# Kernel tuning notes

Measured on AMD Instinct MI355X. Metric: run time of the kernel, lower is better.

The kernel has to match this reference:

```python
import jax, jax.numpy as jnp
import numpy as np

ACT_DIM = 768
DICT_SIZE = 32768
S0 = 4096          # top-level latent size (dict_size // prod(lower sizes))
S1 = 8             # lower_level_latent_sizes[0]
K = 64             # per-token top-k (applied globally as k * batch)


def setup_inputs() -> dict:
    key = jax.random.key(0)
    ks = jax.random.split(key, 7)
    scale_e = 1.0 / np.sqrt(ACT_DIM)
    scale_d = 1.0 / np.sqrt(DICT_SIZE)
    return {
        "x": jax.random.normal(ks[0], (4096, ACT_DIM), dtype=jnp.float32),
        "W0": jax.random.normal(ks[1], (S0, ACT_DIM), dtype=jnp.float32) * scale_e,
        "b0": jnp.zeros((S0,), dtype=jnp.float32),
        "W1": jax.random.normal(ks[2], (DICT_SIZE, ACT_DIM), dtype=jnp.float32) * scale_e,
        "b1": jnp.zeros((DICT_SIZE,), dtype=jnp.float32),
        "Wd": jax.random.normal(ks[3], (ACT_DIM, DICT_SIZE), dtype=jnp.float32) * scale_d,
        "b_dec": jnp.zeros((ACT_DIM,), dtype=jnp.float32),
    }


def reference(x, W0, b0, W1, b1, Wd, b_dec):
    B = x.shape[0]
    x_centered = x - b_dec                                   # [B, D]
    # hierarchical relu encoders
    l0 = jax.nn.relu(x_centered @ W0.T + b0)                 # [B, S0]
    l1 = jax.nn.relu(x_centered @ W1.T + b1)                 # [B, S0*S1]
    # multiplicative gating: lower-level gate broadcast over finest level
    final_dense = (l1.reshape(B, S0, S1) * l0[:, :, None]).reshape(B, S0 * S1)
    # global batch top-k over flattened [B * dict_size]
    flat = final_dense.reshape(-1)
    k_for_batch = min(K * B, flat.shape[0])
    vals, idx = jax.lax.top_k(flat, k_for_batch)
    sparse_flat = jnp.zeros_like(flat).at[idx].set(vals)
    encoded = sparse_flat.reshape(B, S0 * S1)
    # decode
    x_hat = encoded @ Wd.T + b_dec                           # [B, D]
    return x_hat
```

## Files before the change

kernel.cpp:

```cpp
#include <hip/hip_runtime.h>
#include <stdint.h>

#define DDIM 768
#define BROWS 4096
#define S0N 4096
#define DICT 32768
#define KTOT 262144u
#define PREF 2.0f
#define DELTA 4e-3f
#define CAND_CAP 8388608u
#define BAND_CAP 4096

static constexpr size_t OFF_XH   = 0;
static constexpr size_t OFF_XL   = 6291456;
static constexpr size_t OFF_W0H  = 12582912;
static constexpr size_t OFF_W0L  = 18874368;
static constexpr size_t OFF_W1H  = 25165824;
static constexpr size_t OFF_W1L  = 75497472;
static constexpr size_t OFF_WDT  = 0;
static constexpr size_t OFF_L0   = 125829120;
static constexpr size_t OFF_CTRL = 192937984;
static constexpr size_t OFF_ROWC = 193069056;
static constexpr size_t OFF_ROWD = 193085440;
static constexpr size_t OFF_CAND = 201474048;
static constexpr size_t WS_NEED  = 268582912;


typedef __attribute__((ext_vector_type(8))) short bf16x8;
typedef __attribute__((ext_vector_type(4))) float f32x4;

__device__ __forceinline__ unsigned umin_(unsigned a, unsigned b) { return a < b ? a : b; }
__device__ __forceinline__ float relu_(float v) { return v > 0.f ? v : 0.f; }

__device__ __forceinline__ unsigned short f2bf(float f) {
    union { float f; unsigned u; } v; v.f = f;
    unsigned r = v.u + 0x7FFFu + ((v.u >> 16) & 1u);
    return (unsigned short)(r >> 16);
}
__device__ __forceinline__ float bf2f(unsigned short h) {
    union { float f; unsigned u; } v; v.u = ((unsigned)h) << 16;
    return v.f;
}
__device__ __forceinline__ void split1(float a, short& h, short& l) {
    unsigned short hb = f2bf(a);
    float rem = a - bf2f(hb);
    h = (short)hb;
    l = (short)f2bf(rem);
}

__device__ __forceinline__ void gl16(const void* g, void* l) {
    __builtin_amdgcn_global_load_lds(
        (const __attribute__((address_space(1))) void*)g,
        (__attribute__((address_space(3))) void*)l,
        16, 0, 0);
}

__global__ void k_split_x(const float* __restrict__ x, const float* __restrict__ b_dec,
                          short* __restrict__ XH, short* __restrict__ XL) {
    int i = blockIdx.x * 256 + threadIdx.x;
    float4 xv = ((const float4*)x)[i];
    int d = (i % (DDIM / 4)) * 4;
    float4 bv = *(const float4*)(b_dec + d);
    float a[4] = {xv.x - bv.x, xv.y - bv.y, xv.z - bv.z, xv.w - bv.w};
    short4 h, lo;
    split1(a[0], h.x, lo.x); split1(a[1], h.y, lo.y);
    split1(a[2], h.z, lo.z); split1(a[3], h.w, lo.w);
    ((short4*)XH)[i] = h;
    ((short4*)XL)[i] = lo;
}

__global__ void k_split_w(const float* __restrict__ W, short* __restrict__ H,
                          short* __restrict__ L) {
    int i = blockIdx.x * 256 + threadIdx.x;
    float4 wv = ((const float4*)W)[i];
    short4 h, lo;
    split1(wv.x, h.x, lo.x); split1(wv.y, h.y, lo.y);
    split1(wv.z, h.z, lo.z); split1(wv.w, h.w, lo.w);
    ((short4*)H)[i] = h;
    ((short4*)L)[i] = lo;
}

__global__ void k_transpose(const float* __restrict__ Wd, unsigned short* __restrict__ WdT) {
    __shared__ float tile[32][33];
    int j0 = blockIdx.x * 32, d0 = blockIdx.y * 32;
    int tx = threadIdx.x & 31, ty = threadIdx.x >> 5;
#pragma unroll
    for (int i = 0; i < 4; ++i)
        tile[ty + i * 8][tx] = Wd[(size_t)(d0 + ty + i * 8) * DICT + j0 + tx];
    __syncthreads();
#pragma unroll
    for (int i = 0; i < 4; ++i)
        WdT[(size_t)(j0 + ty + i * 8) * DDIM + d0 + tx] = f2bf(tile[tx][ty + i * 8]);
}

template<int EPI>
__launch_bounds__(512, 2) __global__
void k_mm(const short* __restrict__ XH, const short* __restrict__ XL,
          const short* __restrict__ WH, const short* __restrict__ WL,
          const float* __restrict__ bias, float* __restrict__ l0buf,
          uint2* __restrict__ cand, unsigned* __restrict__ ctrl) {
    __shared__ __align__(16) char smem[131072];

    const int t = threadIdx.x;
    const int w = t >> 6, l = t & 63;
    const int wm = w >> 2, wn = w & 3;
    const int lr = l & 15, lk = l >> 4;

    const int nwg = gridDim.x;
    const int bid = blockIdx.x;
    const int swz = (bid & 7) * (nwg >> 3) + (bid >> 3);
    const int bm = (swz & 15) << 8;
    const int bn = (swz >> 4) << 8;

    const int a0 = 2 * w, a1 = a0 + 1;
    const unsigned aB0 = (unsigned)(bm + (a0 >> 3) * 128 + (a0 & 7) * 16 + lr) * 768u + (unsigned)(lk * 8);
    const unsigned aB1 = (unsigned)(bm + (a1 >> 3) * 128 + (a1 & 7) * 16 + lr) * 768u + (unsigned)(lk * 8);
    const unsigned bB0 = (unsigned)(bn + (a0 >> 2) * 64 + (a0 & 3) * 16 + lr) * 768u + (unsigned)(lk * 8);
    const unsigned bB1 = (unsigned)(bn + (a1 >> 2) * 64 + (a1 & 3) * 16 + lr) * 768u + (unsigned)(lk * 8);

    f32x4 acc[8][4];
#pragma unroll
    for (int i = 0; i < 8; ++i)
#pragma unroll
        for (int j = 0; j < 4; ++j) acc[i][j] = (f32x4){0.f, 0.f, 0.f, 0.f};

#pragma unroll
    for (int J = 0; J < 3; ++J) {
        const unsigned kb = (unsigned)J * 32u;
        char* dA = smem + J * 16384 + a0 * 1024;
        char* dB = smem + 65536 + J * 16384 + a0 * 1024;
        gl16(XH + aB0 + kb, dA);
        gl16(XH + aB1 + kb, dA + 1024);
        gl16(WH + bB0 + kb, dB);
        gl16(WH + bB1 + kb, dB + 1024);
    }

#pragma unroll 1
    for (int H = 0; H < 72; ++H) {
        if (H < 70)       asm volatile("s_waitcnt vmcnt(8)" ::: "memory");
        else if (H == 70) asm volatile("s_waitcnt vmcnt(4)" ::: "memory");
        else              asm volatile("s_waitcnt vmcnt(0)" ::: "memory");
        __builtin_amdgcn_s_barrier();

        const char* rA = smem + (H & 3) * 16384;
        const char* rB = smem + 65536 + (H & 3) * 16384;

        const int J = H + 3;
        const short* As = XH; const short* Bs = WH; unsigned kb = 0;
        char* dA = nullptr; char* dB = nullptr;
        const bool hj = J < 72;
        if (hj) {
            const int ktJ = J >> 1;
            if (ktJ < 12)      { As = XH; Bs = WH; kb = (unsigned)ktJ * 64u; }
            else if (ktJ < 24) { As = XH; Bs = WL; kb = (unsigned)(ktJ - 12) * 64u; }
            else               { As = XL; Bs = WH; kb = (unsigned)(ktJ - 24) * 64u; }
            kb += (unsigned)(J & 1) * 32u;
            dA = smem + (J & 3) * 16384 + a0 * 1024;
            dB = smem + 65536 + (J & 3) * 16384 + a0 * 1024;
        }

        bf16x8 bfr[4], af[4];
#pragma unroll
        for (int nj = 0; nj < 4; ++nj)
            bfr[nj] = *(const bf16x8*)(rB + (wn * 4 + nj) * 1024 + l * 16);
#pragma unroll
        for (int m2 = 0; m2 < 4; ++m2)
            af[m2] = *(const bf16x8*)(rA + (wm * 8 + m2) * 1024 + l * 16);
        if (hj) { gl16(As + aB0 + kb, dA); gl16(As + aB1 + kb, dA + 1024); }
        __builtin_amdgcn_sched_barrier(0);
        __builtin_amdgcn_s_barrier();
        asm volatile("s_waitcnt lgkmcnt(0)" ::: "memory");
        __builtin_amdgcn_sched_barrier(0);
        __builtin_amdgcn_s_setprio(1);
#pragma unroll
        for (int m2 = 0; m2 < 4; ++m2)
#pragma unroll
            for (int nj = 0; nj < 4; ++nj)
                acc[m2][nj] = __builtin_amdgcn_mfma_f32_16x16x32_bf16(
                    af[m2], bfr[nj], acc[m2][nj], 0, 0, 0);
        __builtin_amdgcn_s_setprio(0);
        __builtin_amdgcn_s_barrier();

#pragma unroll
        for (int m2 = 0; m2 < 4; ++m2)
            af[m2] = *(const bf16x8*)(rA + (wm * 8 + 4 + m2) * 1024 + l * 16);
        if (hj) { gl16(Bs + bB0 + kb, dB); gl16(Bs + bB1 + kb, dB + 1024); }
        __builtin_amdgcn_sched_barrier(0);
        __builtin_amdgcn_s_barrier();
        asm volatile("s_waitcnt lgkmcnt(0)" ::: "memory");
        __builtin_amdgcn_sched_barrier(0);
        __builtin_amdgcn_s_setprio(1);
#pragma unroll
        for (int m2 = 0; m2 < 4; ++m2)
#pragma unroll
            for (int nj = 0; nj < 4; ++nj)
                acc[4 + m2][nj] = __builtin_amdgcn_mfma_f32_16x16x32_bf16(
                    af[m2], bfr[nj], acc[4 + m2][nj], 0, 0, 0);
        __builtin_amdgcn_s_setprio(0);
        __builtin_amdgcn_s_barrier();
    }
    __syncthreads();

    if constexpr (EPI == 0) {
#pragma unroll
        for (int mi = 0; mi < 8; ++mi) {
#pragma unroll
            for (int r = 0; r < 4; ++r) {
                const int row = bm + wm * 128 + mi * 16 + lk * 4 + r;
                float* orow = l0buf + (size_t)row * S0N;
#pragma unroll
                for (int nj = 0; nj < 4; ++nj) {
                    const int col = bn + wn * 64 + nj * 16 + lr;
                    orow[col] = relu_(acc[mi][nj][r] + bias[col]);
                }
            }
        }
    } else {
        unsigned* pscan = (unsigned*)smem;
        unsigned cnt = 0;
#pragma unroll
        for (int mi = 0; mi < 8; ++mi)
#pragma unroll
            for (int nj = 0; nj < 4; ++nj)
#pragma unroll
                for (int r = 0; r < 4; ++r) {
                    const int row = bm + wm * 128 + mi * 16 + lk * 4 + r;
                    const int col = bn + wn * 64 + nj * 16 + lr;
                    float v = relu_(acc[mi][nj][r] + bias[col]);
                    v *= l0buf[(size_t)row * S0N + (col >> 3)];
                    acc[mi][nj][r] = v;
                    cnt += (v >= PREF) ? 1u : 0u;
                }
        pscan[t] = cnt;
        __syncthreads();
        for (int s = 1; s < 512; s <<= 1) {
            unsigned v2 = (t >= s) ? pscan[t - s] : 0u;
            __syncthreads();
            pscan[t] += v2;
            __syncthreads();
        }
        if (t == 511) pscan[512] = atomicAdd(&ctrl[0], pscan[511]);
        __syncthreads();
        unsigned off = pscan[512] + pscan[t] - cnt;
#pragma unroll
        for (int mi = 0; mi < 8; ++mi)
#pragma unroll
            for (int nj = 0; nj < 4; ++nj)
#pragma unroll
                for (int r = 0; r < 4; ++r) {
                    const float v = acc[mi][nj][r];
                    if (v >= PREF) {
                        const int row = bm + wm * 128 + mi * 16 + lk * 4 + r;
                        const int col = bn + wn * 64 + nj * 16 + lr;
                        if (off < CAND_CAP)
                            cand[off] = make_uint2(__float_as_uint(v),
                                                   ((unsigned)row << 15) | (unsigned)col);
                        ++off;
                    }
                }
    }
}

__global__ void k_hist1(const uint2* __restrict__ cand, unsigned* __restrict__ ctrl) {
    __shared__ unsigned h[2048];
    for (int i = threadIdx.x; i < 2048; i += 256) h[i] = 0;
    __syncthreads();
    unsigned n = umin_(ctrl[0], CAND_CAP);
    for (unsigned i = blockIdx.x * 256 + threadIdx.x; i < n; i += gridDim.x * 256)
        atomicAdd(&h[cand[i].x >> 20], 1u);
    __syncthreads();
    unsigned* hist = ctrl + 256;
    for (int i = threadIdx.x; i < 2048; i += 256)
        if (h[i]) atomicAdd(&hist[i], h[i]);
}

__global__ void k_scan1(unsigned* __restrict__ ctrl) {
    __shared__ unsigned hs[2048];
    __shared__ unsigned cs[256];
    const unsigned* h = ctrl + 256;
    int t = threadIdx.x;
    for (int i = t; i < 2048; i += 256) hs[i] = h[i];
    __syncthreads();
    unsigned s = 0;
    for (int b = 0; b < 8; ++b) s += hs[t * 8 + b];
    cs[t] = s;
    __syncthreads();
    if (t == 0) {
        unsigned cum = 0, T = 0, cb = 0;
        for (int c = 255; c >= 0; --c) {
            if (cum + cs[c] >= KTOT) {
                for (int b = c * 8 + 7; b >= c * 8; --b) {
                    cum += hs[b];
                    if (cum >= KTOT) { T = (unsigned)b; cb = cum - hs[b]; break; }
                }
                break;
            }
            cum += cs[c];
        }
        ctrl[1] = T; ctrl[2] = cb;
    }
}

__global__ void k_hist2(const uint2* __restrict__ cand, unsigned* __restrict__ ctrl) {
    unsigned n = umin_(ctrl[0], CAND_CAP);
    unsigned T = ctrl[1];
    unsigned* hist2 = ctrl + 2304;
    for (unsigned i = blockIdx.x * 256 + threadIdx.x; i < n; i += gridDim.x * 256) {
        unsigned u = cand[i].x;
        if ((u >> 20) == T) atomicAdd(&hist2[(u >> 8) & 0xFFFu], 1u);
    }
}

__global__ void k_scan2(unsigned* __restrict__ ctrl) {
    __shared__ unsigned hs[4096];
    __shared__ unsigned cs[256];
    const unsigned* h = ctrl + 2304;
    int t = threadIdx.x;
    for (int i = t; i < 4096; i += 256) hs[i] = h[i];
    __syncthreads();
    unsigned s = 0;
    for (int b = 0; b < 16; ++b) s += hs[t * 16 + b];
    cs[t] = s;
    __syncthreads();
    if (t == 0) {
        unsigned cum = ctrl[2], T2 = 0;
        for (int c = 255; c >= 0; --c) {
            if (cum + cs[c] >= KTOT) {
                for (int b = c * 16 + 15; b >= c * 16; --b) {
                    cum += hs[b];
                    if (cum >= KTOT) { T2 = (unsigned)b; break; }
                }
                break;
            }
            cum += cs[c];
        }
        ctrl[3] = (ctrl[1] << 12) | T2;
    }
}

__global__ void k_band_rows(const uint2* __restrict__ cand, unsigned* __restrict__ ctrl,
                            unsigned* __restrict__ rowc, uint2* __restrict__ rowd) {
    __shared__ unsigned lhi;
    if (threadIdx.x == 0) lhi = 0;
    __syncthreads();
    unsigned n = umin_(ctrl[0], CAND_CAP);
    unsigned H = ctrl[3];
    float lo = __uint_as_float(H << 8) - DELTA;
    float hi = __uint_as_float((H + 1u) << 8) + DELTA;
    unsigned* band_idx = ctrl + 6400;
    unsigned my = 0;
    for (unsigned i = blockIdx.x * 256 + threadIdx.x; i < n; i += gridDim.x * 256) {
        uint2 cv = cand[i];
        float v = __uint_as_float(cv.x);
        if (v > hi) {
            ++my;
            unsigned b = cv.y >> 15;
            unsigned p = atomicAdd(&rowc[b], 1u);
            if (p < 256u) rowd[(b << 8) + p] = make_uint2(cv.y & 32767u, cv.x);
        } else if (v >= lo) {
            unsigned p = atomicAdd(&ctrl[5], 1u);
            if (p < BAND_CAP) band_idx[p] = cv.y;
        }
    }
    atomicAdd(&lhi, my);
    __syncthreads();
    if (threadIdx.x == 0 && lhi) atomicAdd(&ctrl[4], lhi);
}

__global__ void k_f64(const float* __restrict__ x, const float* __restrict__ b_dec,
                      const float* __restrict__ W0, const float* __restrict__ b0,
                      const float* __restrict__ W1, const float* __restrict__ b1,
                      const unsigned* __restrict__ ctrl, double* __restrict__ band_v) {
    unsigned n = umin_(ctrl[5], BAND_CAP);
    unsigned bi = blockIdx.x;
    if (bi >= n) return;
    const unsigned* band_idx = ctrl + 6400;
    unsigned idx = band_idx[bi];
    int b = idx >> 15, j = idx & 32767, s0 = j >> 3;
    int lane = threadIdx.x;
    const float* xr = x + (size_t)b * DDIM;
    const float* w1 = W1 + (size_t)j * DDIM;
    const float* w0 = W0 + (size_t)s0 * DDIM;
    double d1 = 0.0, d0 = 0.0;
    for (int k = lane; k < DDIM; k += 64) {
        double xv = (double)xr[k] - (double)b_dec[k];
        d1 += xv * (double)w1[k];
        d0 += xv * (double)w0[k];
    }
    for (int off = 32; off; off >>= 1) {
        d1 += __shfl_down(d1, off);
        d0 += __shfl_down(d0, off);
    }
    if (lane == 0) {
        double l1v = d1 + (double)b1[j];  l1v = l1v > 0.0 ? l1v : 0.0;
        double l0v = d0 + (double)b0[s0]; l0v = l0v > 0.0 ? l0v : 0.0;
        band_v[bi] = l1v * l0v;
    }
}

__global__ void k_final(unsigned* __restrict__ ctrl, const double* __restrict__ band_v,
                        uint2* __restrict__ extra) {
    __shared__ unsigned long long skey[BAND_CAP];
    __shared__ unsigned sidx[BAND_CAP];
    int t = threadIdx.x;
    unsigned n = umin_(ctrl[5], BAND_CAP);
    const unsigned* band_idx = ctrl + 6400;
    for (int i = t; i < BAND_CAP; i += 256) {
        if ((unsigned)i < n) {
            skey[i] = (unsigned long long)__double_as_longlong(band_v[i]);
            sidx[i] = band_idx[i];
        } else {
            skey[i] = 0ull; sidx[i] = 0xFFFFFFFFu;
        }
    }
    __syncthreads();
    for (int kk = 2; kk <= BAND_CAP; kk <<= 1) {
        for (int jj = kk >> 1; jj > 0; jj >>= 1) {
            for (int i = t; i < BAND_CAP; i += 256) {
                int ixj = i ^ jj;
                if (ixj > i) {
                    unsigned long long ka = skey[i], kb = skey[ixj];
                    unsigned ia = sidx[i], ib = sidx[ixj];
                    bool ab = (ka > kb) || (ka == kb && ia < ib);
                    bool asc = ((i & kk) == 0);
                    if (asc ? !ab : ab) {
                        skey[i] = kb; skey[ixj] = ka;
                        sidx[i] = ib; sidx[ixj] = ia;
                    }
                }
            }
            __syncthreads();
        }
    }
    unsigned c_hi = ctrl[4];
    unsigned k_rem = (c_hi < KTOT) ? (KTOT - c_hi) : 0u;
    if (k_rem > n) k_rem = n;
    if (t == 0) ctrl[6] = k_rem;
    for (unsigned i = t; i < k_rem; i += 256)
        extra[i] = make_uint2(sidx[i],
                              __float_as_uint((float)__longlong_as_double((long long)skey[i])));
}

__global__ void k_rows_b(const unsigned* __restrict__ ctrl, const uint2* __restrict__ extra,
                         unsigned* __restrict__ rowc, uint2* __restrict__ rowd) {
    unsigned k_rem = ctrl[6];
    for (unsigned i = blockIdx.x * 256 + threadIdx.x; i < k_rem; i += gridDim.x * 256) {
        unsigned idx = extra[i].x;
        unsigned b = idx >> 15;
        unsigned p = atomicAdd(&rowc[b], 1u);
        if (p < 256u) rowd[(b << 8) + p] = make_uint2(idx & 32767u, extra[i].y);
    }
}

__launch_bounds__(192) __global__
void k_decode(const uint2* __restrict__ rowd, const unsigned* __restrict__ rowc,
              const unsigned short* __restrict__ WdT, const float* __restrict__ b_dec,
              float* __restrict__ out) {
    __shared__ uint2 e[256];
    int b = blockIdx.x, t = threadIdx.x;
    unsigned c = rowc[b]; if (c > 256u) c = 256u;
    for (int i = t; i < (int)c; i += 192) e[i] = rowd[(b << 8) + i];
    __syncthreads();
    float4 a = *(const float4*)(b_dec + 4 * t);
#pragma unroll 4
    for (unsigned i = 0; i < c; ++i) {
        float v = __uint_as_float(e[i].y);
        ushort4 w4 = *(const ushort4*)(WdT + (size_t)e[i].x * DDIM + 4 * t);
        a.x = fmaf(v, bf2f(w4.x), a.x);
        a.y = fmaf(v, bf2f(w4.y), a.y);
        a.z = fmaf(v, bf2f(w4.z), a.z);
        a.w = fmaf(v, bf2f(w4.w), a.w);
    }
    *(float4*)(out + (size_t)b * DDIM + 4 * t) = a;
}

extern "C" void kernel_launch(void* const* d_in, const int* in_sizes, int n_in,
                              void* d_out, int out_size, void* d_ws, size_t ws_size,
                              hipStream_t stream) {
    const float* x     = (const float*)d_in[0];
    const float* W0    = (const float*)d_in[1];
    const float* b0    = (const float*)d_in[2];
    const float* W1    = (const float*)d_in[3];
    const float* b1    = (const float*)d_in[4];
    const float* Wd    = (const float*)d_in[5];
    const float* b_dec = (const float*)d_in[6];
    float* out = (float*)d_out;

    if (ws_size < WS_NEED) {
        hipMemsetAsync(d_out, 0, (size_t)out_size * sizeof(float), stream);
        return;
    }

    char* ws = (char*)d_ws;
    short*          XH     = (short*)(ws + OFF_XH);
    short*          XL     = (short*)(ws + OFF_XL);
    short*          W0H    = (short*)(ws + OFF_W0H);
    short*          W0L    = (short*)(ws + OFF_W0L);
    short*          W1H    = (short*)(ws + OFF_W1H);
    short*          W1L    = (short*)(ws + OFF_W1L);
    unsigned short* WdT    = (unsigned short*)(ws + OFF_WDT);
    float*          l0     = (float*)(ws + OFF_L0);
    unsigned*       ctrl   = (unsigned*)(ws + OFF_CTRL);
    double*         band_v = (double*)(ws + OFF_CTRL + 65536);
    uint2*          extra  = (uint2*)(ws + OFF_CTRL + 98304);
    unsigned*       rowc   = (unsigned*)(ws + OFF_ROWC);
    uint2*          rowd   = (uint2*)(ws + OFF_ROWD);
    uint2*          cand   = (uint2*)(ws + OFF_CAND);

    hipMemsetAsync(ctrl, 0, 6400 * sizeof(unsigned), stream);
    hipMemsetAsync(rowc, 0, BROWS * sizeof(unsigned), stream);

    k_split_x<<<(BROWS * DDIM / 4) / 256, 256, 0, stream>>>(x, b_dec, XH, XL);
    k_split_w<<<(S0N * DDIM / 4) / 256, 256, 0, stream>>>(W0, W0H, W0L);
    k_split_w<<<(DICT * DDIM / 4) / 256, 256, 0, stream>>>(W1, W1H, W1L);

    k_mm<0><<<(S0N / 256) * 16, 512, 0, stream>>>(XH, XL, W0H, W0L, b0, l0, nullptr, nullptr);
    k_mm<1><<<(DICT / 256) * 16, 512, 0, stream>>>(XH, XL, W1H, W1L, b1, l0, cand, ctrl);

    k_transpose<<<dim3(DICT / 32, DDIM / 32), 256, 0, stream>>>(Wd, WdT);

    k_hist1<<<1024, 256, 0, stream>>>(cand, ctrl);
    k_scan1<<<1, 256, 0, stream>>>(ctrl);
    k_hist2<<<1024, 256, 0, stream>>>(cand, ctrl);
    k_scan2<<<1, 256, 0, stream>>>(ctrl);
    k_band_rows<<<1024, 256, 0, stream>>>(cand, ctrl, rowc, rowd);
    k_f64<<<BAND_CAP, 64, 0, stream>>>(x, b_dec, W0, b0, W1, b1, ctrl, band_v);
    k_final<<<1, 256, 0, stream>>>(ctrl, band_v, extra);
    k_rows_b<<<32, 256, 0, stream>>>(ctrl, extra, rowc, rowd);

    k_decode<<<BROWS, 192, 0, stream>>>(rowd, rowc, WdT, b_dec, out);
}
```

Measured before the change: 1.143 ms.

## Switch encoder GEMM to 32x32x16 MFMA and shrink bitonic sort to band size

Rewrites the split-bf16 encoder GEMM to use 32x32x16 bf16 MFMA tiles instead of 16x16x32. The global-to-LDS load layout, fragment reads and epilogue row/column mapping change to match. Larger MFMA tiles cut LDS fragment reads per FLOP and the instruction count, at the cost of a more complex accumulator layout. It also sizes the k_final bitonic sort to the next power of two above the band count instead of always 4096, and raises the decode loop unroll.

After: 1.189 ms. +4.0%, slower.

```diff
diff --git a/kernel.cpp b/kernel.cpp
--- a/kernel.cpp
+++ b/kernel.cpp
@@ -27,7 +27,7 @@
 
 
 typedef __attribute__((ext_vector_type(8))) short bf16x8;
-typedef __attribute__((ext_vector_type(4))) float f32x4;
+typedef __attribute__((ext_vector_type(16))) float f32x16;
 
 __device__ __forceinline__ unsigned umin_(unsigned a, unsigned b) { return a < b ? a : b; }
 __device__ __forceinline__ float relu_(float v) { return v > 0.f ? v : 0.f; }
@@ -104,7 +104,7 @@
     const int t = threadIdx.x;
     const int w = t >> 6, l = t & 63;
     const int wm = w >> 2, wn = w & 3;
-    const int lr = l & 15, lk = l >> 4;
+    const int li = l & 31, lh = l >> 5;
 
     const int nwg = gridDim.x;
     const int bid = blockIdx.x;
@@ -112,27 +112,26 @@
     const int bm = (swz & 15) << 8;
     const int bn = (swz >> 4) << 8;
 
-    const int a0 = 2 * w, a1 = a0 + 1;
-    const unsigned aB0 = (unsigned)(bm + (a0 >> 3) * 128 + (a0 & 7) * 16 + lr) * 768u + (unsigned)(lk * 8);
-    const unsigned aB1 = (unsigned)(bm + (a1 >> 3) * 128 + (a1 & 7) * 16 + lr) * 768u + (unsigned)(lk * 8);
-    const unsigned bB0 = (unsigned)(bn + (a0 >> 2) * 64 + (a0 & 3) * 16 + lr) * 768u + (unsigned)(lk * 8);
-    const unsigned bB1 = (unsigned)(bn + (a1 >> 2) * 64 + (a1 & 3) * 16 + lr) * 768u + (unsigned)(lk * 8);
-
-    f32x4 acc[8][4];
-#pragma unroll
-    for (int i = 0; i < 8; ++i)
-#pragma unroll
-        for (int j = 0; j < 4; ++j) acc[i][j] = (f32x4){0.f, 0.f, 0.f, 0.f};
+    const unsigned aB0 = (unsigned)(bm + w * 32 + li) * 768u + (unsigned)(lh * 8);
+    const unsigned bB0 = (unsigned)(bn + w * 32 + li) * 768u + (unsigned)(lh * 8);
+
+    f32x16 acc[4][2];
+#pragma unroll
+    for (int i = 0; i < 4; ++i)
+#pragma unroll
+        for (int j = 0; j < 2; ++j)
+#pragma unroll
+            for (int r = 0; r < 16; ++r) acc[i][j][r] = 0.f;
 
 #pragma unroll
     for (int J = 0; J < 3; ++J) {
         const unsigned kb = (unsigned)J * 32u;
-        char* dA = smem + J * 16384 + a0 * 1024;
-        char* dB = smem + 65536 + J * 16384 + a0 * 1024;
+        char* dA = smem + J * 16384 + 2 * w * 1024;
+        char* dB = smem + 65536 + J * 16384 + 2 * w * 1024;
         gl16(XH + aB0 + kb, dA);
-        gl16(XH + aB1 + kb, dA + 1024);
+        gl16(XH + aB0 + kb + 16, dA + 1024);
         gl16(WH + bB0 + kb, dB);
-        gl16(WH + bB1 + kb, dB + 1024);
+        gl16(WH + bB0 + kb + 16, dB + 1024);
     }
 
 #pragma unroll 1
@@ -155,47 +154,50 @@
             else if (ktJ < 24) { As = XH; Bs = WL; kb = (unsigned)(ktJ - 12) * 64u; }
             else               { As = XL; Bs = WH; kb = (unsigned)(ktJ - 24) * 64u; }
             kb += (unsigned)(J & 1) * 32u;
-            dA = smem + (J & 3) * 16384 + a0 * 1024;
-            dB = smem + 65536 + (J & 3) * 16384 + a0 * 1024;
-        }
-
-        bf16x8 bfr[4], af[4];
-#pragma unroll
-        for (int nj = 0; nj < 4; ++nj)
-            bfr[nj] = *(const bf16x8*)(rB + (wn * 4 + nj) * 1024 + l * 16);
-#pragma unroll
-        for (int m2 = 0; m2 < 4; ++m2)
-            af[m2] = *(const bf16x8*)(rA + (wm * 8 + m2) * 1024 + l * 16);
-        if (hj) { gl16(As + aB0 + kb, dA); gl16(As + aB1 + kb, dA + 1024); }
+            dA = smem + (J & 3) * 16384 + 2 * w * 1024;
+            dB = smem + 65536 + (J & 3) * 16384 + 2 * w * 1024;
+        }
+
+        bf16x8 bfr[2], af[4];
+#pragma unroll
+        for (int nj = 0; nj < 2; ++nj)
+            bfr[nj] = *(const bf16x8*)(rB + ((wn * 2 + nj) * 2 + 0) * 1024 + l * 16);
+#pragma unroll
+        for (int mi = 0; mi < 4; ++mi)
+            af[mi] = *(const bf16x8*)(rA + ((wm * 4 + mi) * 2 + 0) * 1024 + l * 16);
+        if (hj) { gl16(As + aB0 + kb, dA); gl16(As + aB0 + kb + 16, dA + 1024); }
         __builtin_amdgcn_sched_barrier(0);
         __builtin_amdgcn_s_barrier();
         asm volatile("s_waitcnt lgkmcnt(0)" ::: "memory");
         __builtin_amdgcn_sched_barrier(0);
         __builtin_amdgcn_s_setprio(1);
 #pragma unroll
-        for (int m2 = 0; m2 < 4; ++m2)
-#pragma unroll
-            for (int nj = 0; nj < 4; ++nj)
-                acc[m2][nj] = __builtin_amdgcn_mfma_f32_16x16x32_bf16(
-                    af[m2], bfr[nj], acc[m2][nj], 0, 0, 0);
+        for (int mi = 0; mi < 4; ++mi)
+#pragma unroll
+            for (int nj = 0; nj < 2; ++nj)
+                acc[mi][nj] = __builtin_amdgcn_mfma_f32_32x32x16_bf16(
+                    af[mi], bfr[nj], acc[mi][nj], 0, 0, 0);
         __builtin_amdgcn_s_setprio(0);
         __builtin_amdgcn_s_barrier();
 
 #pragma unroll
-        for (int m2 = 0; m2 < 4; ++m2)
-            af[m2] = *(const bf16x8*)(rA + (wm * 8 + 4 + m2) * 1024 + l * 16);
-        if (hj) { gl16(Bs + bB0 + kb, dB); gl16(Bs + bB1 + kb, dB + 1024); }
+        for (int nj = 0; nj < 2; ++nj)
+            bfr[nj] = *(const bf16x8*)(rB + ((wn * 2 + nj) * 2 + 1) * 1024 + l * 16);
+#pragma unroll
+        for (int mi = 0; mi < 4; ++mi)
+            af[mi] = *(const bf16x8*)(rA + ((wm * 4 + mi) * 2 + 1) * 1024 + l * 16);
+        if (hj) { gl16(Bs + bB0 + kb, dB); gl16(Bs + bB0 + kb + 16, dB + 1024); }
         __builtin_amdgcn_sched_barrier(0);
         __builtin_amdgcn_s_barrier();
         asm volatile("s_waitcnt lgkmcnt(0)" ::: "memory");
         __builtin_amdgcn_sched_barrier(0);
         __builtin_amdgcn_s_setprio(1);
 #pragma unroll
-        for (int m2 = 0; m2 < 4; ++m2)
-#pragma unroll
-            for (int nj = 0; nj < 4; ++nj)
-                acc[4 + m2][nj] = __builtin_amdgcn_mfma_f32_16x16x32_bf16(
-                    af[m2], bfr[nj], acc[4 + m2][nj], 0, 0, 0);
+        for (int mi = 0; mi < 4; ++mi)
+#pragma unroll
+            for (int nj = 0; nj < 2; ++nj)
+                acc[mi][nj] = __builtin_amdgcn_mfma_f32_32x32x16_bf16(
+                    af[mi], bfr[nj], acc[mi][nj], 0, 0, 0);
         __builtin_amdgcn_s_setprio(0);
         __builtin_amdgcn_s_barrier();
     }
@@ -203,14 +205,14 @@
 
     if constexpr (EPI == 0) {
 #pragma unroll
-        for (int mi = 0; mi < 8; ++mi) {
-#pragma unroll
-            for (int r = 0; r < 4; ++r) {
-                const int row = bm + wm * 128 + mi * 16 + lk * 4 + r;
+        for (int mi = 0; mi < 4; ++mi) {
+#pragma unroll
+            for (int r = 0; r < 16; ++r) {
+                const int row = bm + wm * 128 + mi * 32 + (r & 3) + 8 * (r >> 2) + 4 * lh;
                 float* orow = l0buf + (size_t)row * S0N;
 #pragma unroll
-                for (int nj = 0; nj < 4; ++nj) {
-                    const int col = bn + wn * 64 + nj * 16 + lr;
+                for (int nj = 0; nj < 2; ++nj) {
+                    const int col = bn + wn * 64 + nj * 32 + li;
                     orow[col] = relu_(acc[mi][nj][r] + bias[col]);
                 }
             }
@@ -219,13 +221,13 @@
         unsigned* pscan = (unsigned*)smem;
         unsigned cnt = 0;
 #pragma unroll
-        for (int mi = 0; mi < 8; ++mi)
-#pragma unroll
-            for (int nj = 0; nj < 4; ++nj)
-#pragma unroll
-                for (int r = 0; r < 4; ++r) {
-                    const int row = bm + wm * 128 + mi * 16 + lk * 4 + r;
-                    const int col = bn + wn * 64 + nj * 16 + lr;
+        for (int mi = 0; mi < 4; ++mi)
+#pragma unroll
+            for (int nj = 0; nj < 2; ++nj)
+#pragma unroll
+                for (int r = 0; r < 16; ++r) {
+                    const int row = bm + wm * 128 + mi * 32 + (r & 3) + 8 * (r >> 2) + 4 * lh;
+                    const int col = bn + wn * 64 + nj * 32 + li;
                     float v = relu_(acc[mi][nj][r] + bias[col]);
                     v *= l0buf[(size_t)row * S0N + (col >> 3)];
                     acc[mi][nj][r] = v;
@@ -243,15 +245,15 @@
         __syncthreads();
         unsigned off = pscan[512] + pscan[t] - cnt;
 #pragma unroll
-        for (int mi = 0; mi < 8; ++mi)
-#pragma unroll
-            for (int nj = 0; nj < 4; ++nj)
-#pragma unroll
-                for (int r = 0; r < 4; ++r) {
+        for (int mi = 0; mi < 4; ++mi)
+#pragma unroll
+            for (int nj = 0; nj < 2; ++nj)
+#pragma unroll
+                for (int r = 0; r < 16; ++r) {
                     const float v = acc[mi][nj][r];
                     if (v >= PREF) {
-                        const int row = bm + wm * 128 + mi * 16 + lk * 4 + r;
-                        const int col = bn + wn * 64 + nj * 16 + lr;
+                        const int row = bm + wm * 128 + mi * 32 + (r & 3) + 8 * (r >> 2) + 4 * lh;
+                        const int col = bn + wn * 64 + nj * 32 + li;
                         if (off < CAND_CAP)
                             cand[off] = make_uint2(__float_as_uint(v),
                                                    ((unsigned)row << 15) | (unsigned)col);
@@ -404,9 +406,10 @@
     __shared__ unsigned sidx[BAND_CAP];
     int t = threadIdx.x;
     unsigned n = umin_(ctrl[5], BAND_CAP);
+    unsigned m = 256; while (m < n) m <<= 1;
     const unsigned* band_idx = ctrl + 6400;
-    for (int i = t; i < BAND_CAP; i += 256) {
-        if ((unsigned)i < n) {
+    for (unsigned i = t; i < m; i += 256) {
+        if (i < n) {
             skey[i] = (unsigned long long)__double_as_longlong(band_v[i]);
             sidx[i] = band_idx[i];
         } else {
@@ -414,10 +417,10 @@
         }
     }
     __syncthreads();
-    for (int kk = 2; kk <= BAND_CAP; kk <<= 1) {
-        for (int jj = kk >> 1; jj > 0; jj >>= 1) {
-            for (int i = t; i < BAND_CAP; i += 256) {
-                int ixj = i ^ jj;
+    for (unsigned kk = 2; kk <= m; kk <<= 1) {
+        for (unsigned jj = kk >> 1; jj > 0; jj >>= 1) {
+            for (unsigned i = t; i < m; i += 256) {
+                unsigned ixj = i ^ jj;
                 if (ixj > i) {
                     unsigned long long ka = skey[i], kb = skey[ixj];
                     unsigned ia = sidx[i], ib = sidx[ixj];
@@ -462,7 +465,7 @@
     for (int i = t; i < (int)c; i += 192) e[i] = rowd[(b << 8) + i];
     __syncthreads();
     float4 a = *(const float4*)(b_dec + 4 * t);
-#pragma unroll 4
+#pragma unroll 8
     for (unsigned i = 0; i < c; ++i) {
         float v = __uint_as_float(e[i].y);
         ushort4 w4 = *(const ushort4*)(WdT + (size_t)e[i].x * DDIM + 4 * t);
```

## Fuse first-pass histogram into gated matmul epilogue and stage gate tile in LDS

Applied to the files above, without the earlier changes.

The gated matmul epilogue now loads the relevant l0 gate tile into shared memory once instead of reading scattered global values per element. It also builds the first radix histogram of candidate values in shared memory and flushes it to global, so the separate k_hist1 pass over the candidate buffer goes away. The final bitonic sort is sized to the next power of two above the band count rather than the full capacity, and the decode loop unroll is raised. The cost is more shared-memory atomics inside the matmul epilogue and extra LDS use, which may affect occupancy.

Result: slower. 1.186 ms (+3.7%).

```diff
diff --git a/kernel.cpp b/kernel.cpp
--- a/kernel.cpp
+++ b/kernel.cpp
@@ -216,7 +216,19 @@
             }
         }
     } else {
-        unsigned* pscan = (unsigned*)smem;
+        float*    gtile = (float*)smem;
+        unsigned* hist  = (unsigned*)(smem + 32768);
+        unsigned* pscan = (unsigned*)(smem + 40960);
+        const int base_s0 = bn >> 3;
+#pragma unroll
+        for (int q = 0; q < 16; ++q) {
+            const int idx = q * 512 + t;
+            const int r = idx >> 5, c = idx & 31;
+            gtile[idx] = l0buf[(size_t)(bm + r) * S0N + base_s0 + c];
+        }
+        for (int i = t; i < 2048; i += 512) hist[i] = 0;
+        __syncthreads();
+
         unsigned cnt = 0;
 #pragma unroll
         for (int mi = 0; mi < 8; ++mi)
@@ -224,12 +236,15 @@
             for (int nj = 0; nj < 4; ++nj)
 #pragma unroll
                 for (int r = 0; r < 4; ++r) {
-                    const int row = bm + wm * 128 + mi * 16 + lk * 4 + r;
-                    const int col = bn + wn * 64 + nj * 16 + lr;
-                    float v = relu_(acc[mi][nj][r] + bias[col]);
-                    v *= l0buf[(size_t)row * S0N + (col >> 3)];
+                    const int lrow = wm * 128 + mi * 16 + lk * 4 + r;
+                    const int lcol = wn * 64 + nj * 16 + lr;
+                    float v = relu_(acc[mi][nj][r] + bias[bn + lcol]);
+                    v *= gtile[lrow * 32 + (lcol >> 3)];
                     acc[mi][nj][r] = v;
-                    cnt += (v >= PREF) ? 1u : 0u;
+                    if (v >= PREF) {
+                        ++cnt;
+                        atomicAdd(&hist[__float_as_uint(v) >> 20], 1u);
+                    }
                 }
         pscan[t] = cnt;
         __syncthreads();
@@ -258,20 +273,10 @@
                         ++off;
                     }
                 }
-    }
-}
-
-__global__ void k_hist1(const uint2* __restrict__ cand, unsigned* __restrict__ ctrl) {
-    __shared__ unsigned h[2048];
-    for (int i = threadIdx.x; i < 2048; i += 256) h[i] = 0;
-    __syncthreads();
-    unsigned n = umin_(ctrl[0], CAND_CAP);
-    for (unsigned i = blockIdx.x * 256 + threadIdx.x; i < n; i += gridDim.x * 256)
-        atomicAdd(&h[cand[i].x >> 20], 1u);
-    __syncthreads();
-    unsigned* hist = ctrl + 256;
-    for (int i = threadIdx.x; i < 2048; i += 256)
-        if (h[i]) atomicAdd(&hist[i], h[i]);
+        unsigned* ghist = ctrl + 256;
+        for (int i = t; i < 2048; i += 512)
+            if (hist[i]) atomicAdd(&ghist[i], hist[i]);
+    }
 }
 
 __global__ void k_scan1(unsigned* __restrict__ ctrl) {
@@ -404,9 +409,10 @@
     __shared__ unsigned sidx[BAND_CAP];
     int t = threadIdx.x;
     unsigned n = umin_(ctrl[5], BAND_CAP);
+    unsigned m = 256; while (m < n) m <<= 1;
     const unsigned* band_idx = ctrl + 6400;
-    for (int i = t; i < BAND_CAP; i += 256) {
-        if ((unsigned)i < n) {
+    for (unsigned i = t; i < m; i += 256) {
+        if (i < n) {
             skey[i] = (unsigned long long)__double_as_longlong(band_v[i]);
             sidx[i] = band_idx[i];
         } else {
@@ -414,10 +420,10 @@
         }
     }
     __syncthreads();
-    for (int kk = 2; kk <= BAND_CAP; kk <<= 1) {
-        for (int jj = kk >> 1; jj > 0; jj >>= 1) {
-            for (int i = t; i < BAND_CAP; i += 256) {
-                int ixj = i ^ jj;
+    for (unsigned kk = 2; kk <= m; kk <<= 1) {
+        for (unsigned jj = kk >> 1; jj > 0; jj >>= 1) {
+            for (unsigned i = t; i < m; i += 256) {
+                unsigned ixj = i ^ jj;
                 if (ixj > i) {
                     unsigned long long ka = skey[i], kb = skey[ixj];
                     unsigned ia = sidx[i], ib = sidx[ixj];
@@ -462,7 +468,7 @@
     for (int i = t; i < (int)c; i += 192) e[i] = rowd[(b << 8) + i];
     __syncthreads();
     float4 a = *(const float4*)(b_dec + 4 * t);
-#pragma unroll 4
+#pragma unroll 8
     for (unsigned i = 0; i < c; ++i) {
         float v = __uint_as_float(e[i].y);
         ushort4 w4 = *(const ushort4*)(WdT + (size_t)e[i].x * DDIM + 4 * t);
@@ -519,7 +525,6 @@
 
     k_transpose<<<dim3(DICT / 32, DDIM / 32), 256, 0, stream>>>(Wd, WdT);
 
-    k_hist1<<<1024, 256, 0, stream>>>(cand, ctrl);
     k_scan1<<<1, 256, 0, stream>>>(ctrl);
     k_hist2<<<1024, 256, 0, stream>>>(cand, ctrl);
     k_scan2<<<1, 256, 0, stream>>>(ctrl);
```

## Shrink GEMM tiles to 128x128 with double buffering and trim band sort

Applied to the files above, without the earlier changes.

Changes the split-bf16 GEMM from 256x256 tiles with 512 threads and a 4-stage LDS ring to 128x128 tiles with 256 threads, a 2-stage buffer, and 4 blocks per CU, aiming for higher occupancy and simpler pipelining. The bitonic sort in the final band kernel now runs only over the next power of two of the actual candidate count instead of the full capacity. The decode loop unroll is also raised. The smaller tiles halve operand reuse per block and increase global/L2 traffic, and the shallower prefetch may expose memory latency.

Result: slower. 1.615 ms (+41.3%).

```diff
diff --git a/kernel.cpp b/kernel.cpp
--- a/kernel.cpp
+++ b/kernel.cpp
@@ -94,119 +94,95 @@
 }
 
 template<int EPI>
-__launch_bounds__(512, 2) __global__
+__launch_bounds__(256, 4) __global__
 void k_mm(const short* __restrict__ XH, const short* __restrict__ XL,
           const short* __restrict__ WH, const short* __restrict__ WL,
           const float* __restrict__ bias, float* __restrict__ l0buf,
           uint2* __restrict__ cand, unsigned* __restrict__ ctrl) {
-    __shared__ __align__(16) char smem[131072];
+    __shared__ __align__(16) char smem[32768];
 
     const int t = threadIdx.x;
     const int w = t >> 6, l = t & 63;
-    const int wm = w >> 2, wn = w & 3;
+    const int wm = w >> 1, wn = w & 1;
     const int lr = l & 15, lk = l >> 4;
 
     const int nwg = gridDim.x;
     const int bid = blockIdx.x;
     const int swz = (bid & 7) * (nwg >> 3) + (bid >> 3);
-    const int bm = (swz & 15) << 8;
-    const int bn = (swz >> 4) << 8;
-
-    const int a0 = 2 * w, a1 = a0 + 1;
-    const unsigned aB0 = (unsigned)(bm + (a0 >> 3) * 128 + (a0 & 7) * 16 + lr) * 768u + (unsigned)(lk * 8);
-    const unsigned aB1 = (unsigned)(bm + (a1 >> 3) * 128 + (a1 & 7) * 16 + lr) * 768u + (unsigned)(lk * 8);
-    const unsigned bB0 = (unsigned)(bn + (a0 >> 2) * 64 + (a0 & 3) * 16 + lr) * 768u + (unsigned)(lk * 8);
-    const unsigned bB1 = (unsigned)(bn + (a1 >> 2) * 64 + (a1 & 3) * 16 + lr) * 768u + (unsigned)(lk * 8);
-
-    f32x4 acc[8][4];
-#pragma unroll
-    for (int i = 0; i < 8; ++i)
+    const int bm = (swz & 31) << 7;
+    const int bn = (swz >> 5) << 7;
+
+    const unsigned aB0 = (unsigned)(bm + 2 * w * 16 + lr) * 768u + (unsigned)(lk * 8);
+    const unsigned aB1 = aB0 + 16u * 768u;
+    const unsigned bB0 = (unsigned)(bn + 2 * w * 16 + lr) * 768u + (unsigned)(lk * 8);
+    const unsigned bB1 = bB0 + 16u * 768u;
+
+    f32x4 acc[4][4];
+#pragma unroll
+    for (int i = 0; i < 4; ++i)
 #pragma unroll
         for (int j = 0; j < 4; ++j) acc[i][j] = (f32x4){0.f, 0.f, 0.f, 0.f};
 
-#pragma unroll
-    for (int J = 0; J < 3; ++J) {
-        const unsigned kb = (unsigned)J * 32u;
-        char* dA = smem + J * 16384 + a0 * 1024;
-        char* dB = smem + 65536 + J * 16384 + a0 * 1024;
-        gl16(XH + aB0 + kb, dA);
-        gl16(XH + aB1 + kb, dA + 1024);
-        gl16(WH + bB0 + kb, dB);
-        gl16(WH + bB1 + kb, dB + 1024);
+    {
+        char* dA = smem + 2 * w * 1024;
+        char* dB = smem + 16384 + 2 * w * 1024;
+        gl16(XH + aB0, dA);
+        gl16(XH + aB1, dA + 1024);
+        gl16(WH + bB0, dB);
+        gl16(WH + bB1, dB + 1024);
     }
 
 #pragma unroll 1
     for (int H = 0; H < 72; ++H) {
-        if (H < 70)       asm volatile("s_waitcnt vmcnt(8)" ::: "memory");
-        else if (H == 70) asm volatile("s_waitcnt vmcnt(4)" ::: "memory");
-        else              asm volatile("s_waitcnt vmcnt(0)" ::: "memory");
         __builtin_amdgcn_s_barrier();
 
-        const char* rA = smem + (H & 3) * 16384;
-        const char* rB = smem + 65536 + (H & 3) * 16384;
-
-        const int J = H + 3;
-        const short* As = XH; const short* Bs = WH; unsigned kb = 0;
-        char* dA = nullptr; char* dB = nullptr;
-        const bool hj = J < 72;
-        if (hj) {
+        const int J = H + 1;
+        if (J < 72) {
+            const short* As; const short* Bs; unsigned kb;
             const int ktJ = J >> 1;
             if (ktJ < 12)      { As = XH; Bs = WH; kb = (unsigned)ktJ * 64u; }
             else if (ktJ < 24) { As = XH; Bs = WL; kb = (unsigned)(ktJ - 12) * 64u; }
             else               { As = XL; Bs = WH; kb = (unsigned)(ktJ - 24) * 64u; }
             kb += (unsigned)(J & 1) * 32u;
-            dA = smem + (J & 3) * 16384 + a0 * 1024;
-            dB = smem + 65536 + (J & 3) * 16384 + a0 * 1024;
-        }
-
-        bf16x8 bfr[4], af[4];
+            char* dA = smem + (J & 1) * 8192 + 2 * w * 1024;
+            char* dB = smem + 16384 + (J & 1) * 8192 + 2 * w * 1024;
+            gl16(As + aB0 + kb, dA);
+            gl16(As + aB1 + kb, dA + 1024);
+            gl16(Bs + bB0 + kb, dB);
+            gl16(Bs + bB1 + kb, dB + 1024);
+            asm volatile("s_waitcnt vmcnt(4)" ::: "memory");
+        } else {
+            asm volatile("s_waitcnt vmcnt(0)" ::: "memory");
+        }
+        __builtin_amdgcn_s_barrier();
+
+        const char* rA = smem + (H & 1) * 8192;
+        const char* rB = smem + 16384 + (H & 1) * 8192;
+        bf16x8 af[4], bfr[4];
+#pragma unroll
+        for (int mi = 0; mi < 4; ++mi)
+            af[mi] = *(const bf16x8*)(rA + (wm * 4 + mi) * 1024 + l * 16);
 #pragma unroll
         for (int nj = 0; nj < 4; ++nj)
             bfr[nj] = *(const bf16x8*)(rB + (wn * 4 + nj) * 1024 + l * 16);
-#pragma unroll
-        for (int m2 = 0; m2 < 4; ++m2)
-            af[m2] = *(const bf16x8*)(rA + (wm * 8 + m2) * 1024 + l * 16);
-        if (hj) { gl16(As + aB0 + kb, dA); gl16(As + aB1 + kb, dA + 1024); }
-        __builtin_amdgcn_sched_barrier(0);
-        __builtin_amdgcn_s_barrier();
+        __builtin_amdgcn_s_setprio(1);
+#pragma unroll
+        for (int mi = 0; mi < 4; ++mi)
+#pragma unroll
+            for (int nj = 0; nj < 4; ++nj)
+                acc[mi][nj] = __builtin_amdgcn_mfma_f32_16x16x32_bf16(
+                    af[mi], bfr[nj], acc[mi][nj], 0, 0, 0);
+        __builtin_amdgcn_s_setprio(0);
         asm volatile("s_waitcnt lgkmcnt(0)" ::: "memory");
-        __builtin_amdgcn_sched_barrier(0);
-        __builtin_amdgcn_s_setprio(1);
-#pragma unroll
-        for (int m2 = 0; m2 < 4; ++m2)
-#pragma unroll
-            for (int nj = 0; nj < 4; ++nj)
-                acc[m2][nj] = __builtin_amdgcn_mfma_f32_16x16x32_bf16(
-                    af[m2], bfr[nj], acc[m2][nj], 0, 0, 0);
-        __builtin_amdgcn_s_setprio(0);
-        __builtin_amdgcn_s_barrier();
-
-#pragma unroll
-        for (int m2 = 0; m2 < 4; ++m2)
-            af[m2] = *(const bf16x8*)(rA + (wm * 8 + 4 + m2) * 1024 + l * 16);
-        if (hj) { gl16(Bs + bB0 + kb, dB); gl16(Bs + bB1 + kb, dB + 1024); }
-        __builtin_amdgcn_sched_barrier(0);
-        __builtin_amdgcn_s_barrier();
-        asm volatile("s_waitcnt lgkmcnt(0)" ::: "memory");
-        __builtin_amdgcn_sched_barrier(0);
-        __builtin_amdgcn_s_setprio(1);
-#pragma unroll
-        for (int m2 = 0; m2 < 4; ++m2)
-#pragma unroll
-            for (int nj = 0; nj < 4; ++nj)
-                acc[4 + m2][nj] = __builtin_amdgcn_mfma_f32_16x16x32_bf16(
-                    af[m2], bfr[nj], acc[4 + m2][nj], 0, 0, 0);
-        __builtin_amdgcn_s_setprio(0);
-        __builtin_amdgcn_s_barrier();
     }
     __syncthreads();
 
     if constexpr (EPI == 0) {
 #pragma unroll
-        for (int mi = 0; mi < 8; ++mi) {
+        for (int mi = 0; mi < 4; ++mi) {
 #pragma unroll
             for (int r = 0; r < 4; ++r) {
-                const int row = bm + wm * 128 + mi * 16 + lk * 4 + r;
+                const int row = bm + wm * 64 + mi * 16 + lk * 4 + r;
                 float* orow = l0buf + (size_t)row * S0N;
 #pragma unroll
                 for (int nj = 0; nj < 4; ++nj) {
@@ -219,12 +195,12 @@
         unsigned* pscan = (unsigned*)smem;
         unsigned cnt = 0;
 #pragma unroll
-        for (int mi = 0; mi < 8; ++mi)
+        for (int mi = 0; mi < 4; ++mi)
 #pragma unroll
             for (int nj = 0; nj < 4; ++nj)
 #pragma unroll
                 for (int r = 0; r < 4; ++r) {
-                    const int row = bm + wm * 128 + mi * 16 + lk * 4 + r;
+                    const int row = bm + wm * 64 + mi * 16 + lk * 4 + r;
                     const int col = bn + wn * 64 + nj * 16 + lr;
                     float v = relu_(acc[mi][nj][r] + bias[col]);
                     v *= l0buf[(size_t)row * S0N + (col >> 3)];
@@ -233,24 +209,24 @@
                 }
         pscan[t] = cnt;
         __syncthreads();
-        for (int s = 1; s < 512; s <<= 1) {
+        for (int s = 1; s < 256; s <<= 1) {
             unsigned v2 = (t >= s) ? pscan[t - s] : 0u;
             __syncthreads();
             pscan[t] += v2;
             __syncthreads();
         }
-        if (t == 511) pscan[512] = atomicAdd(&ctrl[0], pscan[511]);
+        if (t == 255) pscan[256] = atomicAdd(&ctrl[0], pscan[255]);
         __syncthreads();
-        unsigned off = pscan[512] + pscan[t] - cnt;
-#pragma unroll
-        for (int mi = 0; mi < 8; ++mi)
+        unsigned off = pscan[256] + pscan[t] - cnt;
+#pragma unroll
+        for (int mi = 0; mi < 4; ++mi)
 #pragma unroll
             for (int nj = 0; nj < 4; ++nj)
 #pragma unroll
                 for (int r = 0; r < 4; ++r) {
                     const float v = acc[mi][nj][r];
                     if (v >= PREF) {
-                        const int row = bm + wm * 128 + mi * 16 + lk * 4 + r;
+                        const int row = bm + wm * 64 + mi * 16 + lk * 4 + r;
                         const int col = bn + wn * 64 + nj * 16 + lr;
                         if (off < CAND_CAP)
                             cand[off] = make_uint2(__float_as_uint(v),
@@ -404,9 +380,10 @@
     __shared__ unsigned sidx[BAND_CAP];
     int t = threadIdx.x;
     unsigned n = umin_(ctrl[5], BAND_CAP);
+    unsigned m = 256; while (m < n) m <<= 1;
     const unsigned* band_idx = ctrl + 6400;
-    for (int i = t; i < BAND_CAP; i += 256) {
-        if ((unsigned)i < n) {
+    for (unsigned i = t; i < m; i += 256) {
+        if (i < n) {
             skey[i] = (unsigned long long)__double_as_longlong(band_v[i]);
             sidx[i] = band_idx[i];
         } else {
@@ -414,10 +391,10 @@
         }
     }
     __syncthreads();
-    for (int kk = 2; kk <= BAND_CAP; kk <<= 1) {
-        for (int jj = kk >> 1; jj > 0; jj >>= 1) {
-            for (int i = t; i < BAND_CAP; i += 256) {
-                int ixj = i ^ jj;
+    for (unsigned kk = 2; kk <= m; kk <<= 1) {
+        for (unsigned jj = kk >> 1; jj > 0; jj >>= 1) {
+            for (unsigned i = t; i < m; i += 256) {
+                unsigned ixj = i ^ jj;
                 if (ixj > i) {
                     unsigned long long ka = skey[i], kb = skey[ixj];
                     unsigned ia = sidx[i], ib = sidx[ixj];
@@ -462,7 +439,7 @@
     for (int i = t; i < (int)c; i += 192) e[i] = rowd[(b << 8) + i];
     __syncthreads();
     float4 a = *(const float4*)(b_dec + 4 * t);
-#pragma unroll 4
+#pragma unroll 8
     for (unsigned i = 0; i < c; ++i) {
         float v = __uint_as_float(e[i].y);
         ushort4 w4 = *(const ushort4*)(WdT + (size_t)e[i].x * DDIM + 4 * t);
@@ -514,8 +491,8 @@
     k_split_w<<<(S0N * DDIM / 4) / 256, 256, 0, stream>>>(W0, W0H, W0L);
     k_split_w<<<(DICT * DDIM / 4) / 256, 256, 0, stream>>>(W1, W1H, W1L);
 
-    k_mm<0><<<(S0N / 256) * 16, 512, 0, stream>>>(XH, XL, W0H, W0L, b0, l0, nullptr, nullptr);
-    k_mm<1><<<(DICT / 256) * 16, 512, 0, stream>>>(XH, XL, W1H, W1L, b1, l0, cand, ctrl);
+    k_mm<0><<<(S0N / 128) * (BROWS / 128), 256, 0, stream>>>(XH, XL, W0H, W0L, b0, l0, nullptr, nullptr);
+    k_mm<1><<<(DICT / 128) * (BROWS / 128), 256, 0, stream>>>(XH, XL, W1H, W1L, b1, l0, cand, ctrl);
 
     k_transpose<<<dim3(DICT / 32, DDIM / 32), 256, 0, stream>>>(Wd, WdT);
 
```
